# Performance work log

Measured on AMD Instinct MI355X. Metric: run time of the kernel, lower is better.

## Reference

```python
import jax, jax.numpy as jnp
import numpy as np

B, S, D = 4, 2048, 768
H = 12
HD = D // H
SCALE = HD ** -0.5


def setup_inputs() -> dict:
    key = jax.random.key(0)
    ks = jax.random.split(key, 5)
    std = D ** -0.5
    return {
        "hidden_states": jax.random.normal(ks[0], (B, S, D), dtype=jnp.float32),
        "qkv_w": jax.random.normal(ks[1], (3 * D, D), dtype=jnp.float32) * std,
        "qkv_b": jnp.zeros((3 * D,), dtype=jnp.float32),
        "proj_w": jax.random.normal(ks[2], (D, D), dtype=jnp.float32) * std,
        "proj_b": jnp.zeros((D,), dtype=jnp.float32),
    }


def reference(hidden_states, qkv_w, qkv_b, proj_w, proj_b):
    b, s, d = hidden_states.shape
    # fused QKV projection: [b,s,3d] -> [3,b,H,s,hd]
    mixed = hidden_states @ qkv_w.T + qkv_b
    mixed = mixed.reshape(b, s, 3, H, HD).transpose(2, 0, 3, 1, 4)
    q, k, v = mixed[0], mixed[1], mixed[2]
    # naive attention: full [b,H,s,s] score matrix, as in original module
    scores = jnp.einsum("bhqd,bhkd->bhqk", q, k) * SCALE
    probs = jax.nn.softmax(scores, axis=-1)
    ctx = jnp.einsum("bhqk,bhkd->bhqd", probs, v)
    ctx = ctx.transpose(0, 2, 1, 3).reshape(b, s, d)
    out = ctx @ proj_w.T + proj_b
    return out
```

## Files before the change

### kernel.cpp

```cpp
#include <hip/hip_runtime.h>
#include <hip/hip_bf16.h>

using short8  = __attribute__((ext_vector_type(8))) short;
using floatx4 = __attribute__((ext_vector_type(4))) float;

#define KDIM 768
#define QSCALE 0.18033688011112042f

__device__ __forceinline__ short f2bf(float f) {
    union { float f; unsigned u; } v; v.f = f;
    unsigned r = v.u + 0x7fffu + ((v.u >> 16) & 1u);
    return (short)(r >> 16);
}

__device__ __forceinline__ float fast_exp2(float x) {
#if __has_builtin(__builtin_amdgcn_exp2f)
    return __builtin_amdgcn_exp2f(x);
#else
    return exp2f(x);
#endif
}

__device__ __forceinline__ void async16(const void* g, void* l) {
    __builtin_amdgcn_global_load_lds((const __attribute__((address_space(1))) void*)g,
                                     (__attribute__((address_space(3))) void*)l, 16, 0, 0);
}

__global__ void cvt_f32_bf16(const float* __restrict__ in, short* __restrict__ out, int n) {
    int i = (blockIdx.x * blockDim.x + threadIdx.x) * 4;
    if (i >= n) return;
    float4 v = *(const float4*)(in + i);
    short4 o;
    o.x = f2bf(v.x); o.y = f2bf(v.y); o.z = f2bf(v.z); o.w = f2bf(v.w);
    *(short4*)(out + i) = o;
}

__global__ __launch_bounds__(256) void gemm_qkv(
    const short* __restrict__ X, const short* __restrict__ W,
    const float* __restrict__ bias,
    short* __restrict__ Qb, short* __restrict__ Kb, short* __restrict__ Vb)
{
    __shared__ short As[128 * 32];
    __shared__ short Bs[128 * 32];
    int tid = threadIdx.x;
    int w = tid >> 6, l = tid & 63;
    int lane16 = l & 15, quad = l >> 4;
    int wm = w & 1, wn = w >> 1;
    int m0 = blockIdx.y * 128, n0 = blockIdx.x * 128;

    floatx4 acc[4][4] = {};

    int srow = w * 32 + (l >> 2);
    int scol = (l & 3) * 8;
    const short* Xg = X + (size_t)(m0 + srow) * KDIM + scol;
    const short* Wg = W + (size_t)(n0 + srow) * KDIM + scol;
    short* AsW = As + (w * 32) * 32;
    short* BsW = Bs + (w * 32) * 32;

    for (int kb = 0; kb < KDIM; kb += 32) {
        __syncthreads();
        async16(Xg + kb,              AsW);
        async16(Xg + kb + 16 * KDIM,  AsW + 16 * 32);
        async16(Wg + kb,              BsW);
        async16(Wg + kb + 16 * KDIM,  BsW + 16 * 32);
        __syncthreads();
        short8 a[4], b[4];
#pragma unroll
        for (int mt = 0; mt < 4; mt++) a[mt] = *(const short8*)(As + (wm * 64 + mt * 16 + lane16) * 32 + quad * 8);
#pragma unroll
        for (int nt = 0; nt < 4; nt++) b[nt] = *(const short8*)(Bs + (wn * 64 + nt * 16 + lane16) * 32 + quad * 8);
#pragma unroll
        for (int mt = 0; mt < 4; mt++)
#pragma unroll
            for (int nt = 0; nt < 4; nt++)
                acc[mt][nt] = __builtin_amdgcn_mfma_f32_16x16x32_bf16(a[mt], b[nt], acc[mt][nt], 0, 0, 0);
    }

#pragma unroll
    for (int mt = 0; mt < 4; mt++) {
        int row = m0 + wm * 64 + mt * 16 + quad * 4;
#pragma unroll
        for (int nt = 0; nt < 4; nt++) {
            int col = n0 + wn * 64 + nt * 16 + lane16;
            int qkv = (col >= 1536) ? 2 : ((col >= 768) ? 1 : 0);
            int rem = col - qkv * 768;
            int h = rem >> 6, e = rem & 63;
            short* dst = (qkv == 0) ? Qb : ((qkv == 1) ? Kb : Vb);
            float sc = (qkv == 0) ? (float)QSCALE : 1.0f;
            float bv = bias[col];
#pragma unroll
            for (int r = 0; r < 4; r++) {
                int i  = row + r;
                int b_ = i >> 11, s_ = i & 2047;
                dst[(((size_t)(b_ * 12 + h)) * 2048 + s_) * 64 + e] = f2bf((acc[mt][nt][r] + bv) * sc);
            }
        }
    }
}

__global__ __launch_bounds__(256) void transpose_v(
    const short* __restrict__ Vb, short* __restrict__ Vt)
{
    __shared__ short T[64 * 66];
    int tid = threadIdx.x;
    int s0 = blockIdx.x * 64, bh = blockIdx.y;
    const short* src = Vb + (size_t)bh * 2048 * 64;
    short* dst = Vt + (size_t)bh * 64 * 2048;

#pragma unroll
    for (int i = 0; i < 2; i++) {
        int slot = i * 256 + tid;
        int s_loc = slot >> 3, ec = slot & 7;
        short8 v = *(const short8*)(src + (size_t)(s0 + s_loc) * 64 + ec * 8);
        *(short8*)(T + s_loc * 66 + ec * 8) = v;
    }
    __syncthreads();
#pragma unroll
    for (int i = 0; i < 2; i++) {
        int slot = i * 256 + tid;
        int e_loc = slot >> 3, sc = slot & 7;
        short8 o;
#pragma unroll
        for (int j = 0; j < 8; j++) o[j] = T[(sc * 8 + j) * 66 + e_loc];
        *(short8*)(dst + (size_t)e_loc * 2048 + s0 + sc * 8) = o;
    }
}

__global__ __launch_bounds__(256) void attn(
    const short* __restrict__ Qb, const short* __restrict__ Kb,
    const short* __restrict__ Vt, short* __restrict__ Ctx)
{
    __shared__ short Ks[512 * 8];
    __shared__ short Vs[512 * 8];
    __shared__ short Ps[4][128 * 8];
    int tid = threadIdx.x, w = tid >> 6, l = tid & 63;
    int lane16 = l & 15, quad = l >> 4;
    int qt = blockIdx.x, bh = blockIdx.y;
    const short* Qh  = Qb + (size_t)bh * 2048 * 64;
    const short* Kh  = Kb + (size_t)bh * 2048 * 64;
    const short* Vth = Vt + (size_t)bh * 64 * 2048;
    int qbase = qt * 64 + w * 16;
    short* Psw = &Ps[w][0];

    const short* kSrc[2];
    const short* vSrc[2];
    short* kDst[2];
    short* vDst[2];
#pragma unroll
    for (int i = 0; i < 2; i++) {
        int slot = i * 256 + tid;
        int row = slot >> 3;
        int g = (slot & 7) ^ (row & 7);
        kSrc[i] = Kh + (size_t)row * 64 + g * 8;
        vSrc[i] = Vth + (size_t)row * 2048 + g * 8;
        kDst[i] = Ks + (size_t)(i * 256 + w * 64) * 8;
        vDst[i] = Vs + (size_t)(i * 256 + w * 64) * 8;
    }

    short8 qf[2];
#pragma unroll
    for (int kc = 0; kc < 2; kc++)
        qf[kc] = *(const short8*)(Qh + (size_t)(qbase + lane16) * 64 + kc * 32 + quad * 8);

    float lsum[4] = {0.f, 0.f, 0.f, 0.f};
    floatx4 acc[4] = {};

    for (int kt = 0; kt < 32; kt++) {
        __syncthreads();
#pragma unroll
        for (int i = 0; i < 2; i++) {
            async16(kSrc[i] + (size_t)kt * 64 * 64, kDst[i]);
            async16(vSrc[i] + (size_t)kt * 64,      vDst[i]);
        }
        __syncthreads();

        floatx4 s[4];
#pragma unroll
        for (int nt = 0; nt < 4; nt++) {
            floatx4 c = {};
            int row = nt * 16 + lane16;
#pragma unroll
            for (int kc = 0; kc < 2; kc++) {
                int chunk = kc * 4 + quad;
                short8 kf = *(const short8*)(Ks + (size_t)(row * 8 + (chunk ^ (row & 7))) * 8);
                c = __builtin_amdgcn_mfma_f32_16x16x32_bf16(qf[kc], kf, c, 0, 0, 0);
            }
            s[nt] = c;
        }

#pragma unroll
        for (int nt = 0; nt < 4; nt++) {
            int key = nt * 16 + lane16;
            int chunk = key >> 3, pos = key & 7;
#pragma unroll
            for (int r = 0; r < 4; r++) {
                float p = fast_exp2(s[nt][r]);
                lsum[r] += p;
                int row = quad * 4 + r;
                Psw[(row * 8 + (chunk ^ (row & 7))) * 8 + pos] = f2bf(p);
            }
        }

        short8 pa[2];
#pragma unroll
        for (int kc = 0; kc < 2; kc++) {
            int chunk = kc * 4 + quad;
            int row = lane16;
            pa[kc] = *(const short8*)(Psw + (size_t)(row * 8 + (chunk ^ (row & 7))) * 8);
        }
#pragma unroll
        for (int nt = 0; nt < 4; nt++) {
            int row = nt * 16 + lane16;
#pragma unroll
            for (int kc = 0; kc < 2; kc++) {
                int chunk = kc * 4 + quad;
                short8 vf = *(const short8*)(Vs + (size_t)(row * 8 + (chunk ^ (row & 7))) * 8);
                acc[nt] = __builtin_amdgcn_mfma_f32_16x16x32_bf16(pa[kc], vf, acc[nt], 0, 0, 0);
            }
        }
    }

    float inv[4];
#pragma unroll
    for (int r = 0; r < 4; r++) {
        float t = lsum[r];
        t += __shfl_xor(t, 1);
        t += __shfl_xor(t, 2);
        t += __shfl_xor(t, 4);
        t += __shfl_xor(t, 8);
        inv[r] = 1.0f / t;
    }
    int b_ = bh / 12, h = bh % 12;
#pragma unroll
    for (int nt = 0; nt < 4; nt++)
#pragma unroll
        for (int r = 0; r < 4; r++) {
            int q = qbase + quad * 4 + r;
            int e = nt * 16 + lane16;
            Ctx[((size_t)(b_ * 2048 + q)) * 768 + h * 64 + e] = f2bf(acc[nt][r] * inv[r]);
        }
}

__global__ __launch_bounds__(256) void gemm_out(
    const short* __restrict__ Ctx, const short* __restrict__ W,
    const float* __restrict__ bias, float* __restrict__ out)
{
    __shared__ short As[128 * 32];
    __shared__ short Bs[128 * 32];
    int tid = threadIdx.x;
    int w = tid >> 6, l = tid & 63;
    int lane16 = l & 15, quad = l >> 4;
    int wm = w & 1, wn = w >> 1;
    int m0 = blockIdx.y * 128, n0 = blockIdx.x * 128;

    floatx4 acc[4][4] = {};

    int srow = w * 32 + (l >> 2);
    int scol = (l & 3) * 8;
    const short* Xg = Ctx + (size_t)(m0 + srow) * KDIM + scol;
    const short* Wg = W + (size_t)(n0 + srow) * KDIM + scol;
    short* AsW = As + (w * 32) * 32;
    short* BsW = Bs + (w * 32) * 32;

    for (int kb = 0; kb < KDIM; kb += 32) {
        __syncthreads();
        async16(Xg + kb,             AsW);
        async16(Xg + kb + 16 * KDIM, AsW + 16 * 32);
        async16(Wg + kb,             BsW);
        async16(Wg + kb + 16 * KDIM, BsW + 16 * 32);
        __syncthreads();
        short8 a[4], b[4];
#pragma unroll
        for (int mt = 0; mt < 4; mt++) a[mt] = *(const short8*)(As + (wm * 64 + mt * 16 + lane16) * 32 + quad * 8);
#pragma unroll
        for (int nt = 0; nt < 4; nt++) b[nt] = *(const short8*)(Bs + (wn * 64 + nt * 16 + lane16) * 32 + quad * 8);
#pragma unroll
        for (int mt = 0; mt < 4; mt++)
#pragma unroll
            for (int nt = 0; nt < 4; nt++)
                acc[mt][nt] = __builtin_amdgcn_mfma_f32_16x16x32_bf16(a[mt], b[nt], acc[mt][nt], 0, 0, 0);
    }

#pragma unroll
    for (int mt = 0; mt < 4; mt++) {
        int row = m0 + wm * 64 + mt * 16 + quad * 4;
#pragma unroll
        for (int nt = 0; nt < 4; nt++) {
            int col = n0 + wn * 64 + nt * 16 + lane16;
            float bv = bias[col];
#pragma unroll
            for (int r = 0; r < 4; r++)
                out[(size_t)(row + r) * 768 + col] = acc[mt][nt][r] + bv;
        }
    }
}

extern "C" void kernel_launch(void* const* d_in, const int* in_sizes, int n_in,
                              void* d_out, int out_size, void* d_ws, size_t ws_size,
                              hipStream_t stream) {
    const float* hs     = (const float*)d_in[0];
    const float* qkv_w  = (const float*)d_in[1];
    const float* qkv_b  = (const float*)d_in[2];
    const float* proj_w = (const float*)d_in[3];
    const float* proj_b = (const float*)d_in[4];
    float* out = (float*)d_out;

    short* Xb  = (short*)d_ws;
    short* W1b = Xb  + (size_t)8192 * 768;
    short* W2b = W1b + (size_t)2304 * 768;
    short* Qb  = W2b + (size_t)768 * 768;
    short* Kb  = Qb  + (size_t)8192 * 768;
    short* Vb  = Kb  + (size_t)8192 * 768;
    short* Ctx = Vb  + (size_t)8192 * 768;
    short* Vt  = Xb;

    int n1 = 8192 * 768;
    cvt_f32_bf16<<<n1 / 4 / 256, 256, 0, stream>>>(hs, Xb, n1);
    int n2 = 2304 * 768;
    cvt_f32_bf16<<<n2 / 4 / 256, 256, 0, stream>>>(qkv_w, W1b, n2);
    int n3 = 768 * 768;
    cvt_f32_bf16<<<n3 / 4 / 256, 256, 0, stream>>>(proj_w, W2b, n3);

    gemm_qkv<<<dim3(18, 64), 256, 0, stream>>>(Xb, W1b, qkv_b, Qb, Kb, Vb);
    transpose_v<<<dim3(32, 48), 256, 0, stream>>>(Vb, Vt);
    attn<<<dim3(32, 48), 256, 0, stream>>>(Qb, Kb, Vt, Ctx);
    gemm_out<<<dim3(6, 64), 256, 0, stream>>>(Ctx, W2b, proj_b, out);
}
```

Measured before the change: 257.3 us.

## Switch attention to 32x32x16 MFMA with 128-query tiles per block

The attention kernel now uses 32x32x16 bf16 MFMA instructions, and each wave handles 32 query rows instead of 16. The block tile grows to 128 queries, which halves the grid and halves how often K/V tiles are reloaded per query. The P buffer, softmax row-sum reduction and output indexing are reworked for the 32x32 accumulator layout, and launch bounds request 3 blocks per CU. The risks are higher register pressure from the 16-element accumulators, fewer blocks to fill the CUs, and more strided P stores to LDS.

```diff
diff --git a/kernel.cpp b/kernel.cpp
--- a/kernel.cpp
+++ b/kernel.cpp
@@ -1,8 +1,9 @@
 #include <hip/hip_runtime.h>
 #include <hip/hip_bf16.h>
 
-using short8  = __attribute__((ext_vector_type(8))) short;
-using floatx4 = __attribute__((ext_vector_type(4))) float;
+using short8   = __attribute__((ext_vector_type(8))) short;
+using floatx4  = __attribute__((ext_vector_type(4))) float;
+using floatx16 = __attribute__((ext_vector_type(16))) float;
 
 #define KDIM 768
 #define QSCALE 0.18033688011112042f
@@ -11,6 +12,12 @@
     union { float f; unsigned u; } v; v.f = f;
     unsigned r = v.u + 0x7fffu + ((v.u >> 16) & 1u);
     return (short)(r >> 16);
+}
+
+__device__ __forceinline__ unsigned pack2bf(float a, float b) {
+    __hip_bfloat162 h = __float22bfloat162_rn(float2{a, b});
+    union { __hip_bfloat162 h; unsigned u; } c; c.h = h;
+    return c.u;
 }
 
 __device__ __forceinline__ float fast_exp2(float x) {
@@ -126,20 +133,20 @@
     }
 }
 
-__global__ __launch_bounds__(256) void attn(
+__global__ __launch_bounds__(256, 3) void attn(
     const short* __restrict__ Qb, const short* __restrict__ Kb,
     const short* __restrict__ Vt, short* __restrict__ Ctx)
 {
     __shared__ short Ks[512 * 8];
     __shared__ short Vs[512 * 8];
-    __shared__ short Ps[4][128 * 8];
+    __shared__ short Ps[4][256 * 8];
     int tid = threadIdx.x, w = tid >> 6, l = tid & 63;
-    int lane16 = l & 15, quad = l >> 4;
+    int l32 = l & 31, half = l >> 5;
     int qt = blockIdx.x, bh = blockIdx.y;
     const short* Qh  = Qb + (size_t)bh * 2048 * 64;
     const short* Kh  = Kb + (size_t)bh * 2048 * 64;
     const short* Vth = Vt + (size_t)bh * 64 * 2048;
-    int qbase = qt * 64 + w * 16;
+    int qbase = qt * 128 + w * 32;
     short* Psw = &Ps[w][0];
 
     const short* kSrc[2];
@@ -157,13 +164,15 @@
         vDst[i] = Vs + (size_t)(i * 256 + w * 64) * 8;
     }
 
-    short8 qf[2];
-#pragma unroll
-    for (int kc = 0; kc < 2; kc++)
-        qf[kc] = *(const short8*)(Qh + (size_t)(qbase + lane16) * 64 + kc * 32 + quad * 8);
-
-    float lsum[4] = {0.f, 0.f, 0.f, 0.f};
-    floatx4 acc[4] = {};
+    short8 qf[4];
+#pragma unroll
+    for (int ks = 0; ks < 4; ks++)
+        qf[ks] = *(const short8*)(Qh + (size_t)(qbase + l32) * 64 + ks * 16 + half * 8);
+
+    float lsum[16];
+#pragma unroll
+    for (int r = 0; r < 16; r++) lsum[r] = 0.f;
+    floatx16 acc[2] = {};
 
     for (int kt = 0; kt < 32; kt++) {
         __syncthreads();
@@ -174,69 +183,73 @@
         }
         __syncthreads();
 
-        floatx4 s[4];
-#pragma unroll
-        for (int nt = 0; nt < 4; nt++) {
-            floatx4 c = {};
-            int row = nt * 16 + lane16;
-#pragma unroll
-            for (int kc = 0; kc < 2; kc++) {
-                int chunk = kc * 4 + quad;
+        floatx16 s[2];
+#pragma unroll
+        for (int nt = 0; nt < 2; nt++) {
+            floatx16 c = {};
+#pragma unroll
+            for (int ks = 0; ks < 4; ks++) {
+                int row = nt * 32 + l32;
+                int chunk = ks * 2 + half;
                 short8 kf = *(const short8*)(Ks + (size_t)(row * 8 + (chunk ^ (row & 7))) * 8);
-                c = __builtin_amdgcn_mfma_f32_16x16x32_bf16(qf[kc], kf, c, 0, 0, 0);
+                c = __builtin_amdgcn_mfma_f32_32x32x16_bf16(qf[ks], kf, c, 0, 0, 0);
             }
             s[nt] = c;
         }
 
 #pragma unroll
-        for (int nt = 0; nt < 4; nt++) {
-            int key = nt * 16 + lane16;
+        for (int nt = 0; nt < 2; nt++) {
+            int key = nt * 32 + l32;
             int chunk = key >> 3, pos = key & 7;
 #pragma unroll
-            for (int r = 0; r < 4; r++) {
-                float p = fast_exp2(s[nt][r]);
-                lsum[r] += p;
-                int row = quad * 4 + r;
-                Psw[(row * 8 + (chunk ^ (row & 7))) * 8 + pos] = f2bf(p);
+            for (int r = 0; r < 16; r += 2) {
+                float p0 = fast_exp2(s[nt][r]);
+                float p1 = fast_exp2(s[nt][r + 1]);
+                lsum[r]     += p0;
+                lsum[r + 1] += p1;
+                int row0 = (r & 3) + 8 * (r >> 2) + 4 * half;
+                unsigned pk = pack2bf(p0, p1);
+                Psw[(size_t)(row0 * 8 + (chunk ^ (row0 & 7))) * 8 + pos]       = (short)(pk & 0xffff);
+                Psw[(size_t)((row0 + 1) * 8 + (chunk ^ ((row0 + 1) & 7))) * 8 + pos] = (short)(pk >> 16);
             }
         }
 
-        short8 pa[2];
-#pragma unroll
-        for (int kc = 0; kc < 2; kc++) {
-            int chunk = kc * 4 + quad;
-            int row = lane16;
-            pa[kc] = *(const short8*)(Psw + (size_t)(row * 8 + (chunk ^ (row & 7))) * 8);
-        }
-#pragma unroll
-        for (int nt = 0; nt < 4; nt++) {
-            int row = nt * 16 + lane16;
-#pragma unroll
-            for (int kc = 0; kc < 2; kc++) {
-                int chunk = kc * 4 + quad;
+        short8 pa[4];
+#pragma unroll
+        for (int ks = 0; ks < 4; ks++) {
+            int chunk = ks * 2 + half;
+            pa[ks] = *(const short8*)(Psw + (size_t)(l32 * 8 + (chunk ^ (l32 & 7))) * 8);
+        }
+#pragma unroll
+        for (int nt = 0; nt < 2; nt++) {
+#pragma unroll
+            for (int ks = 0; ks < 4; ks++) {
+                int row = nt * 32 + l32;
+                int chunk = ks * 2 + half;
                 short8 vf = *(const short8*)(Vs + (size_t)(row * 8 + (chunk ^ (row & 7))) * 8);
-                acc[nt] = __builtin_amdgcn_mfma_f32_16x16x32_bf16(pa[kc], vf, acc[nt], 0, 0, 0);
+                acc[nt] = __builtin_amdgcn_mfma_f32_32x32x16_bf16(pa[ks], vf, acc[nt], 0, 0, 0);
             }
         }
     }
 
-    float inv[4];
-#pragma unroll
-    for (int r = 0; r < 4; r++) {
+    float inv[16];
+#pragma unroll
+    for (int r = 0; r < 16; r++) {
         float t = lsum[r];
         t += __shfl_xor(t, 1);
         t += __shfl_xor(t, 2);
         t += __shfl_xor(t, 4);
         t += __shfl_xor(t, 8);
+        t += __shfl_xor(t, 16);
         inv[r] = 1.0f / t;
     }
     int b_ = bh / 12, h = bh % 12;
 #pragma unroll
-    for (int nt = 0; nt < 4; nt++)
-#pragma unroll
-        for (int r = 0; r < 4; r++) {
-            int q = qbase + quad * 4 + r;
-            int e = nt * 16 + lane16;
+    for (int nt = 0; nt < 2; nt++)
+#pragma unroll
+        for (int r = 0; r < 16; r++) {
+            int q = qbase + (r & 3) + 8 * (r >> 2) + 4 * half;
+            int e = nt * 32 + l32;
             Ctx[((size_t)(b_ * 2048 + q)) * 768 + h * 64 + e] = f2bf(acc[nt][r] * inv[r]);
         }
 }
@@ -323,6 +336,6 @@
 
     gemm_qkv<<<dim3(18, 64), 256, 0, stream>>>(Xb, W1b, qkv_b, Qb, Kb, Vb);
     transpose_v<<<dim3(32, 48), 256, 0, stream>>>(Vb, Vt);
-    attn<<<dim3(32, 48), 256, 0, stream>>>(Qb, Kb, Vt, Ctx);
+    attn<<<dim3(16, 48), 256, 0, stream>>>(Qb, Kb, Vt, Ctx);
     gemm_out<<<dim3(6, 64), 256, 0, stream>>>(Ctx, W2b, proj_b, out);
 }
```

Result: faster. 238.6 us (-7.3%).
